# Optimization experiments

Measured on AMD Instinct MI355X. Metric: run time of the kernel, lower is better.

Reference implementation:

```python
import jax, jax.numpy as jnp
import numpy as np

NUM_HEADS = 12
DIM = 768
NV = 4  # number of views
EPS = 1e-6


def _ln(x, g, b):
    m = x.mean(-1, keepdims=True)
    v = ((x - m) ** 2).mean(-1, keepdims=True)
    return (x - m) / jnp.sqrt(v + EPS) * g + b


def setup_inputs() -> dict:
    key = jax.random.key(0)
    ks = jax.random.split(key, 10)
    B, N, C, H = 4, 256, DIM, NUM_HEADS
    Hid = 4 * C
    s = 0.02
    return {
        'X': jax.random.normal(ks[0], (B * NV, N, C), jnp.float32),
        'norm1_g': jnp.ones((C,), jnp.float32),
        'norm1_b': jnp.zeros((C,), jnp.float32),
        'qkv_w': jax.random.normal(ks[1], (NV, 3 * C, C), jnp.float32) * s,
        'proj_w': jax.random.normal(ks[2], (NV, C, C), jnp.float32) * s,
        'proj_b': jnp.zeros((NV, C), jnp.float32),
        'norm2_g': jnp.ones((NV, C), jnp.float32),
        'norm2_b': jnp.zeros((NV, C), jnp.float32),
        'fc1_w': jax.random.normal(ks[3], (NV, Hid, C), jnp.float32) * s,
        'fc1_b': jnp.zeros((NV, Hid), jnp.float32),
        'fc2_w': jax.random.normal(ks[4], (NV, C, Hid), jnp.float32) * s,
        'fc2_b': jnp.zeros((NV, C), jnp.float32),
        'query': jax.random.normal(ks[5], (1, 1, C), jnp.float32),
        'mha_in_w': jax.random.normal(ks[6], (NV, 3 * C, C), jnp.float32) * s,
        'mha_in_b': jnp.zeros((NV, 3 * C), jnp.float32),
        'mha_out_w': jax.random.normal(ks[7], (NV, C, C), jnp.float32) * s,
        'mha_out_b': jnp.zeros((NV, C), jnp.float32),
    }


def reference(X, norm1_g, norm1_b, qkv_w, proj_w, proj_b, norm2_g, norm2_b,
              fc1_w, fc1_b, fc2_w, fc2_b, query, mha_in_w, mha_in_b,
              mha_out_w, mha_out_b):
    B4, N, C = X.shape
    B = B4 // NV
    H = NUM_HEADS
    hd = C // H
    scale = hd ** -0.5

    Xv = X.reshape(B, NV, N, C)
    Xn = _ln(Xv, norm1_g, norm1_b)

    # ---- FusionAttention: 4x4 pairwise cross attention between views ----
    qkv = jnp.einsum('bvnc,vdc->vbnd', Xn, qkv_w)              # [V,B,N,3C]
    qkv = qkv.reshape(NV, B, N, 3, H, hd).transpose(3, 0, 1, 4, 2, 5)  # [3,V,B,H,N,hd]
    q, k, v = qkv[0], qkv[1], qkv[2]
    scores = jnp.einsum('ibhnd,jbhmd->ijbhnm', q, k) * scale   # [V,V,B,H,N,N]
    attn = jax.nn.softmax(scores, axis=-1)
    ctx = jnp.einsum('ijbhnm,jbhmd->ijbhnd', attn, v)
    ctx = ctx.transpose(0, 1, 2, 4, 3, 5).reshape(NV, NV, B, N, C)
    # proj_i is affine, so mean over j of proj(x_j) == proj(mean_j x_j)
    ctx_mean = ctx.mean(axis=1)                                # [V,B,N,C]
    xa = jnp.einsum('vbnc,voc->vbno', ctx_mean, proj_w) + proj_b[:, None, None, :]

    x = xa * 2.0
    h = _ln(x, norm2_g[:, None, None, :], norm2_b[:, None, None, :])
    h1 = jax.nn.gelu(jnp.einsum('vbnc,vhc->vbnh', h, fc1_w) + fc1_b[:, None, None, :],
                     approximate=False)
    h2 = jnp.einsum('vbnh,vch->vbnc', h1, fc2_w) + fc2_b[:, None, None, :]
    x = x + h2                                                  # [V,B,N,C]

    # ---- CrossAttentionWithLearnableQuery (query identical for all T,B) ----
    wq, wk, wv = jnp.split(mha_in_w, 3, axis=1)                 # each [V,C,C]
    bq, bk, bv = jnp.split(mha_in_b, 3, axis=1)                 # each [V,C]
    q0 = query.reshape(C)
    qh = (jnp.einsum('c,vdc->vd', q0, wq) + bq).reshape(NV, H, hd)
    kh = (jnp.einsum('vbnc,vdc->vbnd', x, wk) + bk[:, None, None, :]).reshape(NV, B, N, H, hd)
    vh = (jnp.einsum('vbnc,vdc->vbnd', x, wv) + bv[:, None, None, :]).reshape(NV, B, N, H, hd)
    s2 = jnp.einsum('vhd,vbnhd->vbhn', qh, kh) * scale
    a2 = jax.nn.softmax(s2, axis=-1)
    c2 = jnp.einsum('vbhn,vbnhd->vbhd', a2, vh).reshape(NV, B, C)
    o = jnp.einsum('vbc,voc->vbo', c2, mha_out_w) + mha_out_b[:, None, :]  # [V,B,C]
    o = o.transpose(1, 0, 2).reshape(B, NV * C)                 # concat views
    # every query position produces identical output -> broadcast over T=N
    return jnp.broadcast_to(o[:, None, :], (B, N, NV * C))
```

## Files before the change

kernel.cpp:

```cpp
#include <hip/hip_runtime.h>
#include <math.h>

#define NVIEW 4
#define BATCH 4
#define NSEQ  256
#define CDIM  768
#define HEADS 12
#define HD    64

typedef __attribute__((ext_vector_type(8))) short   short8;
typedef __attribute__((ext_vector_type(8))) unsigned short ushort8;
typedef __attribute__((ext_vector_type(4))) float   float4v;

typedef const __attribute__((address_space(1))) void gas_t;
typedef       __attribute__((address_space(3))) void las_t;

__device__ __forceinline__ unsigned short f2b(float x)
{
    union { float f; unsigned u; } c; c.f = x;
    unsigned r = (c.u + 0x7FFFu + ((c.u >> 16) & 1u)) >> 16;
    return (unsigned short)r;
}

__device__ __forceinline__ unsigned pack2b(float a, float b)
{
    return (unsigned)f2b(a) | ((unsigned)f2b(b) << 16);
}

__device__ __forceinline__ ushort8 cvt8(float4 a, float4 b)
{
    union { unsigned u[4]; ushort8 s; } r;
    asm("v_cvt_pk_bf16_f32 %0, %1, %2" : "=v"(r.u[0]) : "v"(a.x), "v"(a.y));
    asm("v_cvt_pk_bf16_f32 %0, %1, %2" : "=v"(r.u[1]) : "v"(a.z), "v"(a.w));
    asm("v_cvt_pk_bf16_f32 %0, %1, %2" : "=v"(r.u[2]) : "v"(b.x), "v"(b.y));
    asm("v_cvt_pk_bf16_f32 %0, %1, %2" : "=v"(r.u[3]) : "v"(b.z), "v"(b.w));
    return r.s;
}

__device__ __forceinline__ void block_ln_row_b(const float* __restrict__ xrow,
                                               const float* __restrict__ g,
                                               const float* __restrict__ b,
                                               unsigned short* __restrict__ orow)
{
    const int t = threadIdx.x;
    float x0 = xrow[t], x1 = xrow[t + 256], x2 = xrow[t + 512];
    float s  = x0 + x1 + x2;
    float s2 = x0 * x0 + x1 * x1 + x2 * x2;
    #pragma unroll
    for (int off = 32; off > 0; off >>= 1) {
        s  += __shfl_down(s, off);
        s2 += __shfl_down(s2, off);
    }
    __shared__ float w1[4], w2[4];
    if ((t & 63) == 0) { w1[t >> 6] = s; w2[t >> 6] = s2; }
    __syncthreads();
    float S  = w1[0] + w1[1] + w1[2] + w1[3];
    float S2 = w2[0] + w2[1] + w2[2] + w2[3];
    float mean = S * (1.0f / 768.0f);
    float var  = S2 * (1.0f / 768.0f) - mean * mean;
    float inv  = rsqrtf(var + 1e-6f);
    orow[t]       = f2b((x0 - mean) * inv * g[t]       + b[t]);
    orow[t + 256] = f2b((x1 - mean) * inv * g[t + 256] + b[t + 256]);
    orow[t + 512] = f2b((x2 - mean) * inv * g[t + 512] + b[t + 512]);
}

__global__ void ln1_kernel(const float* __restrict__ X, const float* __restrict__ g,
                           const float* __restrict__ b, unsigned short* __restrict__ Xn)
{
    int rid = blockIdx.x;
    int n  = rid & 255;
    int bv = rid >> 8;
    int bb = bv >> 2, v = bv & 3;
    const float* xrow = X + (long)rid * CDIM;
    unsigned short* orow = Xn + ((long)(v * 4 + bb) * 256 + n) * CDIM;
    block_ln_row_b(xrow, g, b, orow);
}

__global__ void ln2_kernel(const float* __restrict__ Xin, const float* __restrict__ g,
                           const float* __restrict__ b, unsigned short* __restrict__ Out)
{
    int rid = blockIdx.x;
    int v = rid >> 10;
    const float* xrow = Xin + (long)rid * CDIM;
    block_ln_row_b(xrow, g + v * CDIM, b + v * CDIM, Out + (long)rid * CDIM);
}

template <int EPI, int TM, typename OT>
__launch_bounds__(256, (TM == 128) ? 3 : 4)
__global__ void gemm_bf16(const unsigned short* __restrict__ A,
                          const float* __restrict__ W,
                          const float* __restrict__ bias, const float* __restrict__ resid,
                          OT* __restrict__ out, int M, int N, int K,
                          long wStride, long wOff, int bStride, int bOff)
{
    const int nbx = gridDim.x, nby = gridDim.y;
    const int nwg = nbx * nby * (int)gridDim.z;
    const int orig = blockIdx.x + nbx * (blockIdx.y + nby * blockIdx.z);
    const int cpx = nwg >> 3;
    const int wid = (orig & 7) * cpx + (orig >> 3);
    const int bz  = wid / (nbx * nby);
    const int rr  = wid - bz * (nbx * nby);
    const int by  = rr / nbx;
    const int bx  = rr - by * nbx;

    const int v = bz;
    const unsigned short* Av = A + (long)v * M * K;
    const float* Wv = W + v * wStride + wOff;

    __shared__ unsigned short As[2][TM * 64];
    __shared__ unsigned short Bs[128 * 64];

    const int tid  = threadIdx.x;
    const int lane = tid & 63;
    const int wave = tid >> 6;
    const int l15  = lane & 15;
    const int quad = lane >> 4;
    const int row0 = by * TM, col0 = bx * 128;

    constexpr int MI = 4;
    constexpr int NI = (TM == 128) ? 4 : 2;
    const int mw = (TM == 128) ? (wave & 1) * 64 : 0;
    const int nw = (TM == 128) ? (wave >> 1) * 64 : wave * 32;

    float4v acc[MI][NI];
    #pragma unroll
    for (int i = 0; i < MI; ++i)
        #pragma unroll
        for (int j = 0; j < NI; ++j)
            acc[i][j] = (float4v){0.f, 0.f, 0.f, 0.f};

    const int lr8 = lane >> 3;
    const int p8  = lane & 7;

    auto STAGEA = [&](int buf, int k0) {
        #pragma unroll
        for (int g = 0; g < TM / 32; ++g) {
            int G = wave * (TM / 32) + g;
            int r = G * 8 + lr8;
            int c = p8 ^ (r & 7);
            const unsigned short* sa = Av + (long)(row0 + r) * K + k0 + c * 8;
            __builtin_amdgcn_global_load_lds((gas_t*)sa, (las_t*)&As[buf][G * 512], 16, 0, 0);
        }
    };

    const int brow = tid >> 3;
    const int bch  = tid & 7;
    float4 bp[8];
    auto LOADB = [&](int k0) {
        #pragma unroll
        for (int it = 0; it < 4; ++it) {
            const float* s = Wv + (long)(col0 + it * 32 + brow) * K + k0 + bch * 8;
            bp[it * 2]     = *(const float4*)s;
            bp[it * 2 + 1] = *(const float4*)(s + 4);
        }
    };

    const int NK = K >> 6;
    STAGEA(0, 0);
    LOADB(0);

    for (int t = 0; t < NK; ++t) {
        asm volatile("s_waitcnt vmcnt(0)" ::: "memory");
        __builtin_amdgcn_s_barrier();
        __builtin_amdgcn_sched_barrier(0);

        #pragma unroll
        for (int it = 0; it < 4; ++it) {
            ushort8 o = cvt8(bp[it * 2], bp[it * 2 + 1]);
            int r = it * 32 + brow;
            *(ushort8*)&Bs[r * 64 + (bch ^ (r & 7)) * 8] = o;
        }
        if (t + 1 < NK) {
            STAGEA((t + 1) & 1, (t + 1) * 64);
            LOADB((t + 1) * 64);
        }
        asm volatile("s_waitcnt lgkmcnt(0)" ::: "memory");
        __builtin_amdgcn_s_barrier();
        __builtin_amdgcn_sched_barrier(0);

        const unsigned short* Ac = As[t & 1];
        #pragma unroll
        for (int ks = 0; ks < 2; ++ks) {
            short8 af[MI], bfr[NI];
            #pragma unroll
            for (int mi = 0; mi < MI; ++mi) {
                int m = mw + mi * 16 + l15;
                int p = (ks * 4 + quad) ^ (m & 7);
                af[mi] = *(const short8*)&Ac[m * 64 + p * 8];
            }
            #pragma unroll
            for (int ni = 0; ni < NI; ++ni) {
                int n = nw + ni * 16 + l15;
                int p = (ks * 4 + quad) ^ (n & 7);
                bfr[ni] = *(const short8*)&Bs[n * 64 + p * 8];
            }
            #pragma unroll
            for (int mi = 0; mi < MI; ++mi)
                #pragma unroll
                for (int ni = 0; ni < NI; ++ni)
                    acc[mi][ni] = __builtin_amdgcn_mfma_f32_16x16x32_bf16(af[mi], bfr[ni], acc[mi][ni], 0, 0, 0);
        }
    }

    #pragma unroll
    for (int mi = 0; mi < MI; ++mi) {
        #pragma unroll
        for (int ni = 0; ni < NI; ++ni) {
            int rowb = row0 + mw + mi * 16 + quad * 4;
            int col  = col0 + nw + ni * 16 + l15;
            float bval = 0.f;
            if (EPI >= 1) bval = bias[v * bStride + bOff + col];
            #pragma unroll
            for (int r = 0; r < 4; ++r) {
                float x = acc[mi][ni][r] + bval;
                long off = (long)v * M * N + (long)(rowb + r) * N + col;
                if constexpr (EPI == 2) {
                    x = 0.5f * x * (1.0f + erff(x * 0.70710678118654752f));
                } else if constexpr (EPI == 3) {
                    x += resid[off];
                } else if constexpr (EPI == 4) {
                    x *= 2.0f;
                }
                if constexpr (sizeof(OT) == 2) ((unsigned short*)out)[off] = f2b(x);
                else                           ((float*)out)[off] = x;
            }
        }
    }
}

__launch_bounds__(256, 3)
__global__ void fusion_attn_mfma(const unsigned short* __restrict__ QKV,
                                 unsigned short* __restrict__ ctx)
{
    const int qt = blockIdx.x;
    const int b  = blockIdx.y / HEADS;
    const int h  = blockIdx.y % HEADS;
    const int i  = blockIdx.z;
    const int tid  = threadIdx.x;
    const int lane = tid & 63;
    const int wave = tid >> 6;
    const int l15  = lane & 15;
    const int quad = lane >> 4;

    __shared__ unsigned short Qs[64 * 72];
    __shared__ unsigned short KVu[64 * 136];
    __shared__ unsigned short Ps[64 * 136];

    {
        int r = tid >> 2, p16 = (tid & 3) * 16;
        const unsigned short* src = QKV + ((long)((i * 4 + b) * 256 + qt * 64 + r)) * 2304 + h * 64 + p16;
        *(ushort8*)(&Qs[r * 72 + p16])     = *(const ushort8*)(src);
        *(ushort8*)(&Qs[r * 72 + p16 + 8]) = *(const ushort8*)(src + 8);
    }

    const int kg = tid & 31;
    const int dc = tid >> 5;

    float4v acc_o[4];
    #pragma unroll
    for (int e = 0; e < 4; ++e) acc_o[e] = (float4v){0.f, 0.f, 0.f, 0.f};

    for (int j = 0; j < 4; ++j) {
        const unsigned short* Kb = QKV + ((long)((j * 4 + b) * 256)) * 2304 + 768 + h * 64;
        const unsigned short* Vb = Kb + 768;

        float4v sacc[16];
        #pragma unroll
        for (int t = 0; t < 16; ++t) sacc[t] = (float4v){0.f, 0.f, 0.f, 0.f};

        ushort8 vv0[4], vv1[4];

        __syncthreads();
        #pragma unroll
        for (int g = 0; g < 4; ++g) {
            int R = wave * 32 + g * 8;
            int r = R + (lane >> 3);
            int p = lane & 7;
            int c = (p - (r & 7)) & 7;
            const unsigned short* src = Kb + (long)(r) * 2304 + c * 8;
            __builtin_amdgcn_global_load_lds((gas_t*)src, (las_t*)&KVu[R * 64], 16, 0, 0);
        }
        __syncthreads();
        __builtin_amdgcn_s_setprio(1);
        #pragma unroll
        for (int ks = 0; ks < 2; ++ks) {
            int lcq = ks * 4 + quad;
            short8 qf = *(const short8*)&Qs[(wave * 16 + l15) * 72 + lcq * 8];
            #pragma unroll
            for (int nn = 0; nn < 8; ++nn) {
                int n = nn * 16 + l15;
                int p = (lcq + (n & 7)) & 7;
                short8 kf = *(const short8*)&KVu[n * 64 + p * 8];
                sacc[nn] = __builtin_amdgcn_mfma_f32_16x16x32_bf16(kf, qf, sacc[nn], 0, 0, 0);
            }
        }
        __builtin_amdgcn_s_setprio(0);

        __syncthreads();
        #pragma unroll
        for (int g = 0; g < 4; ++g) {
            int R = wave * 32 + g * 8;
            int r = R + (lane >> 3);
            int p = lane & 7;
            int c = (p - (r & 7)) & 7;
            const unsigned short* src = Kb + (long)(128 + r) * 2304 + c * 8;
            __builtin_amdgcn_global_load_lds((gas_t*)src, (las_t*)&KVu[R * 64], 16, 0, 0);
        }
        __builtin_amdgcn_sched_barrier(0);
        #pragma unroll
        for (int q = 0; q < 4; ++q)
            vv0[q] = *(const ushort8*)(Vb + (long)(kg * 4 + q) * 2304 + dc * 8);
        asm volatile("s_waitcnt vmcnt(4) lgkmcnt(0)" ::: "memory");
        __builtin_amdgcn_s_barrier();
        __builtin_amdgcn_sched_barrier(0);
        __builtin_amdgcn_s_setprio(1);
        #pragma unroll
        for (int ks = 0; ks < 2; ++ks) {
            int lcq = ks * 4 + quad;
            short8 qf = *(const short8*)&Qs[(wave * 16 + l15) * 72 + lcq * 8];
            #pragma unroll
            for (int nn = 0; nn < 8; ++nn) {
                int n = nn * 16 + l15;
                int p = (lcq + (n & 7)) & 7;
                short8 kf = *(const short8*)&KVu[n * 64 + p * 8];
                sacc[8 + nn] = __builtin_amdgcn_mfma_f32_16x16x32_bf16(kf, qf, sacc[8 + nn], 0, 0, 0);
            }
        }
        __builtin_amdgcn_s_setprio(0);

        float m = -1e30f;
        #pragma unroll
        for (int t = 0; t < 16; ++t)
            #pragma unroll
            for (int r = 0; r < 4; ++r) {
                sacc[t][r] *= 0.125f;
                m = fmaxf(m, sacc[t][r]);
            }
        m = fmaxf(m, __shfl_xor(m, 16));
        m = fmaxf(m, __shfl_xor(m, 32));
        float lsum = 0.f;
        #pragma unroll
        for (int t = 0; t < 16; ++t)
            #pragma unroll
            for (int r = 0; r < 4; ++r) {
                float e = __expf(sacc[t][r] - m);
                sacc[t][r] = e;
                lsum += e;
            }
        lsum += __shfl_xor(lsum, 16);
        lsum += __shfl_xor(lsum, 32);
        float invl = 1.0f / lsum;

        float4v pv[4];
        #pragma unroll
        for (int e = 0; e < 4; ++e) pv[e] = (float4v){0.f, 0.f, 0.f, 0.f};

        __syncthreads();
        #pragma unroll
        for (int nn = 0; nn < 8; ++nn) {
            unsigned lo = pack2b(sacc[nn][0], sacc[nn][1]);
            unsigned hi = pack2b(sacc[nn][2], sacc[nn][3]);
            *(unsigned long long*)&Ps[(wave * 16 + l15) * 136 + nn * 16 + quad * 4] =
                ((unsigned long long)hi << 32) | lo;
        }
        #pragma unroll
        for (int jj = 0; jj < 8; ++jj) {
            unsigned lo = (unsigned)vv0[0][jj] | ((unsigned)vv0[1][jj] << 16);
            unsigned hi = (unsigned)vv0[2][jj] | ((unsigned)vv0[3][jj] << 16);
            *(unsigned long long*)&KVu[(dc * 8 + jj) * 136 + kg * 4] =
                ((unsigned long long)hi << 32) | lo;
        }
        #pragma unroll
        for (int q = 0; q < 4; ++q)
            vv1[q] = *(const ushort8*)(Vb + (long)(128 + kg * 4 + q) * 2304 + dc * 8);
        asm volatile("s_waitcnt lgkmcnt(0)" ::: "memory");
        __builtin_amdgcn_s_barrier();
        __builtin_amdgcn_sched_barrier(0);
        __builtin_amdgcn_s_setprio(1);
        #pragma unroll
        for (int ks = 0; ks < 4; ++ks) {
            int lc = ks * 4 + quad;
            short8 pf = *(const short8*)&Ps[(wave * 16 + l15) * 136 + lc * 8];
            #pragma unroll
            for (int et = 0; et < 4; ++et) {
                short8 vf = *(const short8*)&KVu[(et * 16 + l15) * 136 + lc * 8];
                pv[et] = __builtin_amdgcn_mfma_f32_16x16x32_bf16(vf, pf, pv[et], 0, 0, 0);
            }
        }
        __builtin_amdgcn_s_setprio(0);

        __syncthreads();
        #pragma unroll
        for (int nn = 0; nn < 8; ++nn) {
            unsigned lo = pack2b(sacc[8 + nn][0], sacc[8 + nn][1]);
            unsigned hi = pack2b(sacc[8 + nn][2], sacc[8 + nn][3]);
            *(unsigned long long*)&Ps[(wave * 16 + l15) * 136 + nn * 16 + quad * 4] =
                ((unsigned long long)hi << 32) | lo;
        }
        #pragma unroll
        for (int jj = 0; jj < 8; ++jj) {
            unsigned lo = (unsigned)vv1[0][jj] | ((unsigned)vv1[1][jj] << 16);
            unsigned hi = (unsigned)vv1[2][jj] | ((unsigned)vv1[3][jj] << 16);
            *(unsigned long long*)&KVu[(dc * 8 + jj) * 136 + kg * 4] =
                ((unsigned long long)hi << 32) | lo;
        }
        __syncthreads();
        __builtin_amdgcn_s_setprio(1);
        #pragma unroll
        for (int ks = 0; ks < 4; ++ks) {
            int lc = ks * 4 + quad;
            short8 pf = *(const short8*)&Ps[(wave * 16 + l15) * 136 + lc * 8];
            #pragma unroll
            for (int et = 0; et < 4; ++et) {
                short8 vf = *(const short8*)&KVu[(et * 16 + l15) * 136 + lc * 8];
                pv[et] = __builtin_amdgcn_mfma_f32_16x16x32_bf16(vf, pf, pv[et], 0, 0, 0);
            }
        }
        __builtin_amdgcn_s_setprio(0);

        #pragma unroll
        for (int et = 0; et < 4; ++et)
            #pragma unroll
            for (int r = 0; r < 4; ++r)
                acc_o[et][r] += pv[et][r] * invl;
    }

    #pragma unroll
    for (int et = 0; et < 4; ++et) {
        unsigned lo = pack2b(acc_o[et][0] * 0.25f, acc_o[et][1] * 0.25f);
        unsigned hi = pack2b(acc_o[et][2] * 0.25f, acc_o[et][3] * 0.25f);
        long row = (long)((i * 4 + b) * 256 + qt * 64 + wave * 16 + l15);
        int  col = h * 64 + et * 16 + quad * 4;
        *(unsigned long long*)&ctx[row * 768 + col] = ((unsigned long long)hi << 32) | lo;
    }
}

__launch_bounds__(256, 4)
__global__ void qh_kernel(const float* __restrict__ query, const float* __restrict__ Win,
                          const float* __restrict__ Bin, float* __restrict__ QH)
{
    const int bi   = blockIdx.x;
    const int v    = bi / 192;
    const int dblk = bi - v * 192;
    const int t    = threadIdx.x;
    const int wave = t >> 6;
    const int lane = t & 63;
    const int d    = dblk * 4 + wave;

    __shared__ float qs[768];
    for (int idx = t; idx < 768; idx += 256) qs[idx] = query[idx];
    __syncthreads();

    const float* w = Win + ((long)v * 2304 + d) * 768;
    float acc = 0.f;
    #pragma unroll
    for (int k = 0; k < 3; ++k) {
        int c = k * 256 + lane * 4;
        float4 w4 = *(const float4*)(w + c);
        float4 q4 = *(const float4*)&qs[c];
        acc += w4.x * q4.x + w4.y * q4.y + w4.z * q4.z + w4.w * q4.w;
    }
    #pragma unroll
    for (int off = 32; off > 0; off >>= 1) acc += __shfl_down(acc, off);
    if (lane == 0)
        QH[v * 768 + d] = acc + Bin[(long)v * 2304 + d];
}

__launch_bounds__(256, 2)
__global__ void cross_attn(const float* __restrict__ KVH, const float* __restrict__ QH,
                           float* __restrict__ C2)
{
    const int h = blockIdx.x, b = blockIdx.y, v = blockIdx.z;
    const int t = threadIdx.x;
    __shared__ float qv[64];
    __shared__ float p[256];
    __shared__ float part[4][64];
    __shared__ float wred[4], wred2[4];

    if (t < 64) qv[t] = QH[(v * 12 + h) * 64 + t];
    __syncthreads();

    const float* krow = KVH + ((long)((v * 4 + b) * 256 + t)) * 1536 + h * 64;
    float s = 0.f;
    #pragma unroll
    for (int e = 0; e < 64; e += 4) {
        float4 k4 = *(const float4*)(krow + e);
        s += qv[e] * k4.x + qv[e + 1] * k4.y + qv[e + 2] * k4.z + qv[e + 3] * k4.w;
    }
    s *= 0.125f;
    float m4 = s;
    #pragma unroll
    for (int off = 32; off > 0; off >>= 1) m4 = fmaxf(m4, __shfl_down(m4, off));
    if ((t & 63) == 0) wred[t >> 6] = m4;
    __syncthreads();
    float rmax = fmaxf(fmaxf(wred[0], wred[1]), fmaxf(wred[2], wred[3]));
    float ev = __expf(s - rmax);
    p[t] = ev;
    float s4 = ev;
    #pragma unroll
    for (int off = 32; off > 0; off >>= 1) s4 += __shfl_down(s4, off);
    if ((t & 63) == 0) wred2[t >> 6] = s4;
    __syncthreads();
    float inv = 1.0f / (wred2[0] + wred2[1] + wred2[2] + wred2[3]);

    const int e = t & 63, ch = t >> 6;
    const float* vbase = KVH + ((long)((v * 4 + b) * 256)) * 1536 + 768 + h * 64 + e;
    float accv = 0.f;
    for (int m = ch * 64; m < ch * 64 + 64; ++m)
        accv += p[m] * vbase[(long)m * 1536];
    part[ch][e] = accv;
    __syncthreads();
    if (t < 64)
        C2[(v * 4 + b) * 768 + h * 64 + t] =
            (part[0][t] + part[1][t] + part[2][t] + part[3][t]) * inv;
}

__launch_bounds__(256, 4)
__global__ void out_matvec(const float* __restrict__ C2, const float* __restrict__ Wout,
                           const float* __restrict__ Bout, float* __restrict__ obc)
{
    const int bi   = blockIdx.x;
    const int v    = bi / 192;
    const int dblk = bi - v * 192;
    const int t    = threadIdx.x;
    const int wave = t >> 6;
    const int lane = t & 63;
    const int d    = dblk * 4 + wave;

    __shared__ float c2s[3072];
    #pragma unroll
    for (int idx = 0; idx < 3072; idx += 256) c2s[idx + t] = C2[v * 3072 + idx + t];
    __syncthreads();

    const float* w = Wout + ((long)v * 768 + d) * 768;
    float acc0 = 0.f, acc1 = 0.f, acc2 = 0.f, acc3 = 0.f;
    #pragma unroll
    for (int k = 0; k < 3; ++k) {
        int c = k * 256 + lane * 4;
        float4 w4 = *(const float4*)(w + c);
        float4 a0 = *(const float4*)&c2s[c];
        float4 a1 = *(const float4*)&c2s[768 + c];
        float4 a2 = *(const float4*)&c2s[1536 + c];
        float4 a3 = *(const float4*)&c2s[2304 + c];
        acc0 += w4.x * a0.x + w4.y * a0.y + w4.z * a0.z + w4.w * a0.w;
        acc1 += w4.x * a1.x + w4.y * a1.y + w4.z * a1.z + w4.w * a1.w;
        acc2 += w4.x * a2.x + w4.y * a2.y + w4.z * a2.z + w4.w * a2.w;
        acc3 += w4.x * a3.x + w4.y * a3.y + w4.z * a3.z + w4.w * a3.w;
    }
    #pragma unroll
    for (int off = 32; off > 0; off >>= 1) {
        acc0 += __shfl_down(acc0, off);
        acc1 += __shfl_down(acc1, off);
        acc2 += __shfl_down(acc2, off);
        acc3 += __shfl_down(acc3, off);
    }
    if (lane == 0) {
        float bb = Bout[v * 768 + d];
        obc[0 * 3072 + v * 768 + d] = acc0 + bb;
        obc[1 * 3072 + v * 768 + d] = acc1 + bb;
        obc[2 * 3072 + v * 768 + d] = acc2 + bb;
        obc[3 * 3072 + v * 768 + d] = acc3 + bb;
    }
}

__launch_bounds__(256, 4)
__global__ void out_bcast(const float* __restrict__ obc, float* __restrict__ out)
{
    const int b  = blockIdx.x >> 6;
    const int n0 = (blockIdx.x & 63) * 4;
    const int t  = threadIdx.x;
    const float4* src = (const float4*)(obc + (long)b * 3072);
    float4 v0 = src[t], v1 = src[t + 256], v2 = src[t + 512];
    float4* dst = (float4*)(out + ((long)(b * 256 + n0)) * 3072);
    #pragma unroll
    for (int r = 0; r < 4; ++r) {
        dst[r * 768 + t]       = v0;
        dst[r * 768 + t + 256] = v1;
        dst[r * 768 + t + 512] = v2;
    }
}

extern "C" void kernel_launch(void* const* d_in, const int* in_sizes, int n_in,
                              void* d_out, int out_size, void* d_ws, size_t ws_size,
                              hipStream_t stream)
{
    const float* X        = (const float*)d_in[0];
    const float* n1g      = (const float*)d_in[1];
    const float* n1b      = (const float*)d_in[2];
    const float* qkv_w    = (const float*)d_in[3];
    const float* proj_w   = (const float*)d_in[4];
    const float* proj_b   = (const float*)d_in[5];
    const float* n2g      = (const float*)d_in[6];
    const float* n2b      = (const float*)d_in[7];
    const float* fc1_w    = (const float*)d_in[8];
    const float* fc1_b    = (const float*)d_in[9];
    const float* fc2_w    = (const float*)d_in[10];
    const float* fc2_b    = (const float*)d_in[11];
    const float* query    = (const float*)d_in[12];
    const float* mha_in_w = (const float*)d_in[13];
    const float* mha_in_b = (const float*)d_in[14];
    const float* mha_out_w= (const float*)d_in[15];
    const float* mha_out_b= (const float*)d_in[16];
    float* out = (float*)d_out;

    char* wsb = (char*)d_ws;
    unsigned short* rgA  = (unsigned short*)(wsb + 18874368);
    char*           rgB  = wsb + 25165824;
    float*          xbuf = (float*)(wsb + 50331648);
    float*          qh   = (float*)(wsb + 62914560);
    float*          c2   = (float*)(wsb + 62926848);
    float*          obc  = (float*)(wsb + 62976000);

    unsigned short* QKV = (unsigned short*)rgB;
    unsigned short* H1  = (unsigned short*)rgB;
    float*          KVH = (float*)rgB;

    ln1_kernel<<<4096, 256, 0, stream>>>(X, n1g, n1b, rgA);
    gemm_bf16<0, 128, unsigned short><<<dim3(18, 8, 4), 256, 0, stream>>>(
        rgA, qkv_w, nullptr, nullptr, QKV, 1024, 2304, 768, 2304L * 768, 0, 0, 0);
    fusion_attn_mfma<<<dim3(4, 48, 4), 256, 0, stream>>>(QKV, rgA);
    gemm_bf16<4, 64, float><<<dim3(6, 16, 4), 256, 0, stream>>>(
        rgA, proj_w, proj_b, nullptr, xbuf, 1024, 768, 768, 768L * 768, 0, 768, 0);
    ln2_kernel<<<4096, 256, 0, stream>>>(xbuf, n2g, n2b, rgA);
    gemm_bf16<2, 128, unsigned short><<<dim3(24, 8, 4), 256, 0, stream>>>(
        rgA, fc1_w, fc1_b, nullptr, H1, 1024, 3072, 768, 3072L * 768, 0, 3072, 0);
    gemm_bf16<3, 64, unsigned short><<<dim3(6, 16, 4), 256, 0, stream>>>(
        H1, fc2_w, fc2_b, xbuf, rgA, 1024, 768, 3072, 768L * 3072, 0, 768, 0);
    gemm_bf16<1, 64, float><<<dim3(12, 16, 4), 256, 0, stream>>>(
        rgA, mha_in_w, mha_in_b, nullptr, KVH, 1024, 1536, 768, 2304L * 768, 768L * 768, 2304, 768);
    qh_kernel<<<768, 256, 0, stream>>>(query, mha_in_w, mha_in_b, qh);
    cross_attn<<<dim3(12, 4, 4), 256, 0, stream>>>(KVH, qh, c2);
    out_matvec<<<768, 256, 0, stream>>>(c2, mha_out_w, mha_out_b, obc);
    out_bcast<<<256, 256, 0, stream>>>(obc, out);
}
```

Baseline: 435.3 us.

## Deepen GEMM prefetch to two k-tiles with triple-buffered A and double B registers

Restructures the bf16 GEMM main loop so global loads run two k-steps ahead. A gets triple-buffered LDS and B uses two register sets, with partial vmcnt waits instead of draining all loads each iteration. This aims to hide global memory latency behind MFMA work. In exchange it raises register and LDS usage, and occupancy hints are lowered to match. The loop assumes an even number of k-tiles, and the vmcnt counts are hand-tuned.

```diff
diff --git a/kernel.cpp b/kernel.cpp
--- a/kernel.cpp
+++ b/kernel.cpp
@@ -86,7 +86,7 @@
 }
 
 template <int EPI, int TM, typename OT>
-__launch_bounds__(256, (TM == 128) ? 3 : 4)
+__launch_bounds__(256, (TM == 128) ? 2 : 3)
 __global__ void gemm_bf16(const unsigned short* __restrict__ A,
                           const float* __restrict__ W,
                           const float* __restrict__ bias, const float* __restrict__ resid,
@@ -107,7 +107,7 @@
     const unsigned short* Av = A + (long)v * M * K;
     const float* Wv = W + v * wStride + wOff;
 
-    __shared__ unsigned short As[2][TM * 64];
+    __shared__ unsigned short As[3][TM * 64];
     __shared__ unsigned short Bs[128 * 64];
 
     const int tid  = threadIdx.x;
@@ -131,6 +131,10 @@
 
     const int lr8 = lane >> 3;
     const int p8  = lane & 7;
+    const int brow = tid >> 3;
+    const int bch  = tid & 7;
+
+    float4 bpA[8], bpB[8];
 
     auto STAGEA = [&](int buf, int k0) {
         #pragma unroll
@@ -142,11 +146,7 @@
             __builtin_amdgcn_global_load_lds((gas_t*)sa, (las_t*)&As[buf][G * 512], 16, 0, 0);
         }
     };
-
-    const int brow = tid >> 3;
-    const int bch  = tid & 7;
-    float4 bp[8];
-    auto LOADB = [&](int k0) {
+    auto LOADB = [&](float4* bp, int k0) {
         #pragma unroll
         for (int it = 0; it < 4; ++it) {
             const float* s = Wv + (long)(col0 + it * 32 + brow) * K + k0 + bch * 8;
@@ -154,31 +154,15 @@
             bp[it * 2 + 1] = *(const float4*)(s + 4);
         }
     };
-
-    const int NK = K >> 6;
-    STAGEA(0, 0);
-    LOADB(0);
-
-    for (int t = 0; t < NK; ++t) {
-        asm volatile("s_waitcnt vmcnt(0)" ::: "memory");
-        __builtin_amdgcn_s_barrier();
-        __builtin_amdgcn_sched_barrier(0);
-
+    auto WRITEB = [&](const float4* bp) {
         #pragma unroll
         for (int it = 0; it < 4; ++it) {
-            ushort8 o = cvt8(bp[it * 2], bp[it * 2 + 1]);
+            ushort8 ov = cvt8(bp[it * 2], bp[it * 2 + 1]);
             int r = it * 32 + brow;
-            *(ushort8*)&Bs[r * 64 + (bch ^ (r & 7)) * 8] = o;
-        }
-        if (t + 1 < NK) {
-            STAGEA((t + 1) & 1, (t + 1) * 64);
-            LOADB((t + 1) * 64);
-        }
-        asm volatile("s_waitcnt lgkmcnt(0)" ::: "memory");
-        __builtin_amdgcn_s_barrier();
-        __builtin_amdgcn_sched_barrier(0);
-
-        const unsigned short* Ac = As[t & 1];
+            *(ushort8*)&Bs[r * 64 + (bch ^ (r & 7)) * 8] = ov;
+        }
+    };
+    auto COMPUTE = [&](const unsigned short* Ac) {
         #pragma unroll
         for (int ks = 0; ks < 2; ++ks) {
             short8 af[MI], bfr[NI];
@@ -200,6 +184,42 @@
                 for (int ni = 0; ni < NI; ++ni)
                     acc[mi][ni] = __builtin_amdgcn_mfma_f32_16x16x32_bf16(af[mi], bfr[ni], acc[mi][ni], 0, 0, 0);
         }
+    };
+
+    const int NK = K >> 6;
+    STAGEA(0, 0);  LOADB(bpA, 0);
+    STAGEA(1, 64); LOADB(bpB, 64);
+
+    for (int tt = 0; tt < (NK >> 1); ++tt) {
+        const int e = tt * 2, o = e + 1;
+
+        if constexpr (TM == 128) asm volatile("s_waitcnt vmcnt(12)" ::: "memory");
+        else                     asm volatile("s_waitcnt vmcnt(10)" ::: "memory");
+        __builtin_amdgcn_s_barrier();
+        __builtin_amdgcn_sched_barrier(0);
+        WRITEB(bpA);
+        if (e + 2 < NK) { STAGEA((e + 2) % 3, (e + 2) * 64); LOADB(bpA, (e + 2) * 64); }
+        asm volatile("s_waitcnt lgkmcnt(0)" ::: "memory");
+        __builtin_amdgcn_sched_barrier(0);
+        __builtin_amdgcn_s_barrier();
+        __builtin_amdgcn_sched_barrier(0);
+        COMPUTE(As[e % 3]);
+
+        if (o + 1 < NK) {
+            if constexpr (TM == 128) asm volatile("s_waitcnt vmcnt(12)" ::: "memory");
+            else                     asm volatile("s_waitcnt vmcnt(10)" ::: "memory");
+        } else {
+            asm volatile("s_waitcnt vmcnt(0)" ::: "memory");
+        }
+        __builtin_amdgcn_s_barrier();
+        __builtin_amdgcn_sched_barrier(0);
+        WRITEB(bpB);
+        if (o + 2 < NK) { STAGEA((o + 2) % 3, (o + 2) * 64); LOADB(bpB, (o + 2) * 64); }
+        asm volatile("s_waitcnt lgkmcnt(0)" ::: "memory");
+        __builtin_amdgcn_sched_barrier(0);
+        __builtin_amdgcn_s_barrier();
+        __builtin_amdgcn_sched_barrier(0);
+        COMPUTE(As[o % 3]);
     }
 
     #pragma unroll
```

New measurement: 457.1 us. 1.05x slower.
